# Performance work log

Hardware: AMD Instinct MI355X
Metric: run time of the kernel (lower is better)

The kernel has to match this reference:

```python
import jax, jax.numpy as jnp
import numpy as np

N, D_IN, HID, NH = 16384, 2048, 2048, 16
HD = HID // NH  # head_size = 128


def setup_inputs() -> dict:
    key = jax.random.key(0)
    ks = jax.random.split(key, 8)
    s = 1.0 / np.sqrt(D_IN)
    return {
        "protein": jax.random.normal(ks[0], (N, D_IN), jnp.float32),
        "drug": jax.random.normal(ks[1], (N, D_IN), jnp.float32),
        "mask_prot": jnp.ones((N,), bool),
        "mask_drug": jnp.ones((N,), bool),
        "Wq_p": jax.random.uniform(ks[2], (D_IN, HID), jnp.float32, -s, s),
        "Wk_p": jax.random.uniform(ks[3], (D_IN, HID), jnp.float32, -s, s),
        "Wv_p": jax.random.uniform(ks[4], (D_IN, HID), jnp.float32, -s, s),
        "Wq_d": jax.random.uniform(ks[5], (D_IN, HID), jnp.float32, -s, s),
        "Wk_d": jax.random.uniform(ks[6], (D_IN, HID), jnp.float32, -s, s),
        "Wv_d": jax.random.uniform(ks[7], (D_IN, HID), jnp.float32, -s, s),
    }


def _heads(x):
    # [N, L, HID] -> [N, L, NH, HD]
    return x.reshape(x.shape[0], x.shape[1], NH, HD)


def _alpha_logits(logits, mask_row, mask_col, inf=1e6):
    # logits: [N, L1, L2, H]; masks: [N, L1], [N, L2] (broadcast over heads)
    mask_pair = mask_row[:, :, None, None] & mask_col[:, None, :, None]
    logits = jnp.where(mask_pair, logits, logits - inf)
    alpha = jax.nn.softmax(logits, axis=2)
    alpha = jnp.where(mask_row[:, :, None, None], alpha, jnp.zeros_like(alpha))
    return alpha


def reference(protein, drug, mask_prot, mask_drug, Wq_p, Wk_p, Wv_p, Wq_d, Wk_d, Wv_d):
    p = protein[:, None, :]  # [N, 1, D_IN]
    d = drug[:, None, :]
    # forward() overwrites the masks with all-ones of shape [N, L=1]
    m_p = jnp.ones(p.shape[:-1], bool)
    m_d = jnp.ones(d.shape[:-1], bool)

    qp = _heads(jnp.einsum('bld,dh->blh', p, Wq_p))  # [N,1,NH,HD]
    kp = _heads(jnp.einsum('bld,dh->blh', p, Wk_p))
    vp = _heads(jnp.einsum('bld,dh->blh', p, Wv_p))
    qd = _heads(jnp.einsum('bld,dh->blh', d, Wq_d))
    kd = _heads(jnp.einsum('bld,dh->blh', d, Wk_d))
    vd = _heads(jnp.einsum('bld,dh->blh', d, Wv_d))

    logits_pp = jnp.einsum('blhd,bkhd->blkh', qp, kp)
    logits_pd = jnp.einsum('blhd,bkhd->blkh', qp, kd)
    logits_dp = jnp.einsum('blhd,bkhd->blkh', qd, kp)
    logits_dd = jnp.einsum('blhd,bkhd->blkh', qd, kd)

    a_pp = _alpha_logits(logits_pp, m_p, m_p)
    a_pd = _alpha_logits(logits_pd, m_p, m_d)
    a_dp = _alpha_logits(logits_dp, m_d, m_p)
    a_dd = _alpha_logits(logits_dd, m_d, m_d)

    def agg(alpha, v):
        out = jnp.einsum('blkh,bkhd->blhd', alpha, v)
        return out.reshape(out.shape[0], out.shape[1], HID)

    prot_embedding = (agg(a_pp, vp) + agg(a_pd, vd)) / 2  # [N,1,HID]
    drug_embedding = (agg(a_dp, vp) + agg(a_dd, vd)) / 2

    # agg_mode == 'cls'
    prot_embed = prot_embedding[:, 0]
    drug_embed = drug_embedding[:, 0]
    return jnp.concatenate([prot_embed, drug_embed], axis=1)  # [N, 2*HID]
```

## Files before the change

kernel.cpp:

```cpp
#include <hip/hip_runtime.h>
#include <stdint.h>


typedef __attribute__((ext_vector_type(8))) short short8;
typedef __attribute__((ext_vector_type(4))) float float4v;
typedef __attribute__((ext_vector_type(2))) unsigned int uint2v;

typedef const __attribute__((address_space(1))) unsigned int* gp_t;
typedef __attribute__((address_space(3))) unsigned int* lp_t;

#define M_DIM 16384
#define N_DIM 2048
#define K_DIM 4096
#define OUT_LD 4096

static __device__ __forceinline__ unsigned int pack_bf16x2(float x, float y) {
  union { float f; unsigned int u; } a, b;
  a.f = x; b.f = y;
  unsigned int ua = a.u + 0x8000u;
  unsigned int ub = b.u + 0x8000u;
  return __builtin_amdgcn_perm(ub, ua, 0x07060302u);
}

static __device__ __forceinline__ unsigned short f2bf(float x) {
  union { float f; unsigned int u; } a; a.f = x;
  return (unsigned short)((a.u + 0x8000u) >> 16);
}

__global__ __launch_bounds__(256)
void prep_wt(const float* __restrict__ Wp, const float* __restrict__ Wd,
             unsigned short* __restrict__ Wt) {
  __shared__ float tile[32][33];
  const int k0 = blockIdx.x * 32;
  const int n0 = blockIdx.y * 32;
  const int tx = threadIdx.x;
  const int ty = threadIdx.y;
  const float* W = (k0 < 2048) ? Wp : Wd;
  const int kk0 = (k0 < 2048) ? k0 : k0 - 2048;
#pragma unroll
  for (int i = 0; i < 4; ++i) {
    int r = ty * 4 + i;
    tile[r][tx] = W[(size_t)(kk0 + r) * 2048 + n0 + tx];
  }
  __syncthreads();
#pragma unroll
  for (int i = 0; i < 4; ++i) {
    int r = ty * 4 + i;
    Wt[(size_t)(n0 + r) * (size_t)K_DIM + k0 + tx] = f2bf(tile[tx][r]);
  }
}

__global__ __launch_bounds__(256)
void cast_a(const float* __restrict__ P, const float* __restrict__ Dg,
            unsigned int* __restrict__ Abf) {
  int idx = blockIdx.x * 256 + threadIdx.x;
  int row = idx >> 10;
  int j = (idx & 1023) << 2;
  const float* src = (j < 2048) ? (P + (size_t)row * 2048 + j)
                                : (Dg + (size_t)row * 2048 + (j - 2048));
  float4v v = *(const float4v*)src;
  uint2v o;
  o.x = pack_bf16x2(v.x, v.y);
  o.y = pack_bf16x2(v.z, v.w);
  *(uint2v*)(Abf + (size_t)row * 2048 + (j >> 1)) = o;
}

template <bool ABF>
__global__ __launch_bounds__(256)
void gemm_k(const unsigned int* __restrict__ Abf,
            const float* __restrict__ Ap, const float* __restrict__ Ad,
            const unsigned short* __restrict__ Wt,
            float* __restrict__ out) {
  __shared__ unsigned short As[128 * 64];
  __shared__ unsigned short Bs[128 * 64];

  const int t = threadIdx.x;
  const int bx = blockIdx.x;
  const int tn = bx & 15, tm = bx >> 4;
  const int m0 = tm << 7, n0 = tn << 7;
  const int w = t >> 6, l = t & 63;
  const int wm = w & 1, wn = w >> 1;
  const int lr = l & 15, q = l >> 4;

  const int rB = t >> 3;
  const int kB = (t & 7) * 8;

  float4v acc[4][4];
#pragma unroll
  for (int i = 0; i < 4; ++i)
#pragma unroll
    for (int j = 0; j < 4; ++j)
      acc[i][j] = (float4v){0.f, 0.f, 0.f, 0.f};

  for (int k0 = 0; k0 < K_DIM; k0 += 64) {
#pragma unroll
    for (int i = 0; i < 4; ++i) {
      const unsigned short* g =
          Wt + (size_t)(n0 + i * 32 + rB) * (size_t)K_DIM + (k0 + kB);
      __builtin_amdgcn_global_load_lds((gp_t)(const void*)g,
                                       (lp_t)&Bs[i * 2048 + w * 512], 16, 0, 0);
    }
    if constexpr (ABF) {
#pragma unroll
      for (int i = 0; i < 4; ++i) {
        const unsigned int* g =
            Abf + ((size_t)(m0 + i * 32 + rB) * (size_t)K_DIM + (k0 + kB)) / 2;
        __builtin_amdgcn_global_load_lds((gp_t)(const void*)g,
                                         (lp_t)&As[i * 2048 + w * 512], 16, 0, 0);
      }
    } else {
      const float* base;
      int kk;
      if (k0 < 2048) { base = Ap; kk = k0; } else { base = Ad; kk = k0 - 2048; }
      const int rA = t >> 4;
      const int cA = (t & 15) * 4;
#pragma unroll
      for (int i = 0; i < 8; ++i) {
        int m = i * 16 + rA;
        float4v v = *(const float4v*)(base + (size_t)(m0 + m) * 2048 + kk + cA);
        uint2v o;
        o.x = pack_bf16x2(v.x, v.y);
        o.y = pack_bf16x2(v.z, v.w);
        *(uint2v*)&As[m * 64 + cA] = o;
      }
    }
    __syncthreads();

#pragma unroll
    for (int ks = 0; ks < 2; ++ks) {
      short8 af[4], bfr[4];
#pragma unroll
      for (int i = 0; i < 4; ++i) {
        af[i]  = *(const short8*)&As[(wm * 64 + i * 16 + lr) * 64 + ks * 32 + q * 8];
        bfr[i] = *(const short8*)&Bs[(wn * 64 + i * 16 + lr) * 64 + ks * 32 + q * 8];
      }
#pragma unroll
      for (int i = 0; i < 4; ++i)
#pragma unroll
        for (int j = 0; j < 4; ++j)
          acc[i][j] = __builtin_amdgcn_mfma_f32_16x16x32_bf16(af[i], bfr[j],
                                                              acc[i][j], 0, 0, 0);
    }
    __syncthreads();
  }

#pragma unroll
  for (int i = 0; i < 4; ++i) {
    const int r0 = m0 + wm * 64 + i * 16 + q * 4;
#pragma unroll
    for (int j = 0; j < 4; ++j) {
      const int c = n0 + wn * 64 + j * 16 + lr;
#pragma unroll
      for (int r = 0; r < 4; ++r) {
        float v = acc[i][j][r] * 0.5f;
        size_t o = (size_t)(r0 + r) * (size_t)OUT_LD + c;
        out[o] = v;
        out[o + 2048] = v;
      }
    }
  }
}

__global__ __launch_bounds__(256)
void gemm_fallback(const float* __restrict__ P, const float* __restrict__ Dg,
                   const float* __restrict__ Wp, const float* __restrict__ Wd,
                   float* __restrict__ out) {
  __shared__ float Asf[64][17];
  __shared__ float Bsf[16][65];
  const int bx = blockIdx.x;
  const int by = blockIdx.y;
  const int t = threadIdx.x;
  const int tc = t & 15, trw = t >> 4;
  const int m0 = by * 64, n0 = bx * 64;
  float accf[4][4] = {};
  for (int k0 = 0; k0 < 4096; k0 += 16) {
    const float* Asrc = (k0 < 2048) ? P : Dg;
    const float* Bsrc = (k0 < 2048) ? Wp : Wd;
    const int kk = k0 & 2047;
#pragma unroll
    for (int i = 0; i < 4; ++i) {
      int r = i * 16 + trw;
      Asf[r][tc] = Asrc[(size_t)(m0 + r) * 2048 + kk + tc];
    }
#pragma unroll
    for (int i = 0; i < 4; ++i) {
      int r = i * 4 + (t >> 6);
      int c = t & 63;
      Bsf[r][c] = Bsrc[(size_t)(kk + r) * 2048 + n0 + c];
    }
    __syncthreads();
#pragma unroll
    for (int k2 = 0; k2 < 16; ++k2) {
      float a[4], b[4];
#pragma unroll
      for (int i = 0; i < 4; ++i) a[i] = Asf[trw * 4 + i][k2];
#pragma unroll
      for (int j = 0; j < 4; ++j) b[j] = Bsf[k2][tc * 4 + j];
#pragma unroll
      for (int i = 0; i < 4; ++i)
#pragma unroll
        for (int j = 0; j < 4; ++j) accf[i][j] += a[i] * b[j];
    }
    __syncthreads();
  }
#pragma unroll
  for (int i = 0; i < 4; ++i)
#pragma unroll
    for (int j = 0; j < 4; ++j) {
      float v = accf[i][j] * 0.5f;
      size_t o = (size_t)(m0 + trw * 4 + i) * 4096 + n0 + tc * 4 + j;
      out[o] = v;
      out[o + 2048] = v;
    }
}

extern "C" void kernel_launch(void* const* d_in, const int* in_sizes, int n_in,
                              void* d_out, int out_size, void* d_ws, size_t ws_size,
                              hipStream_t stream) {
  const float* protein = (const float*)d_in[0];
  const float* drug    = (const float*)d_in[1];
  const float* Wv_p    = (const float*)d_in[6];
  const float* Wv_d    = (const float*)d_in[9];
  float* out = (float*)d_out;

  const size_t wt_bytes = (size_t)N_DIM * K_DIM * sizeof(unsigned short);
  const size_t a_bytes  = (size_t)M_DIM * K_DIM * sizeof(unsigned short);

  if (ws_size >= wt_bytes) {
    unsigned short* Wt = (unsigned short*)d_ws;
    prep_wt<<<dim3(128, 64), dim3(32, 8), 0, stream>>>(Wv_p, Wv_d, Wt);
    if (ws_size >= wt_bytes + a_bytes) {
      unsigned int* Abf = (unsigned int*)((char*)d_ws + wt_bytes);
      cast_a<<<65536, 256, 0, stream>>>(protein, drug, Abf);
      gemm_k<true><<<2048, 256, 0, stream>>>(Abf, nullptr, nullptr, Wt, out);
    } else {
      gemm_k<false><<<2048, 256, 0, stream>>>(nullptr, protein, drug, Wt, out);
    }
  } else {
    gemm_fallback<<<dim3(32, 256), 256, 0, stream>>>(protein, drug, Wv_p, Wv_d, out);
  }
}
```

Before: 828.6 us.

## Fuse A fp32-to-bf16 cast into GEMM and XOR-swizzle LDS tiles

Drops the separate cast_a kernel and its bf16 A workspace round trip. The GEMM now loads fp32 A directly, converts it in registers and writes 16-byte chunks to LDS. Both the A and B LDS tiles use an XOR swizzle on the 8-element column chunk to avoid bank conflicts on the MFMA fragment reads. prep_wt now writes packed 4-element bf16 stores. The trade-off is that every output-column tile block reloads A as fp32, doubling A read traffic from L2/HBM, and A loads are synchronous rather than async global_load_lds.

```diff
diff --git a/kernel.cpp b/kernel.cpp
--- a/kernel.cpp
+++ b/kernel.cpp
@@ -5,6 +5,7 @@
 typedef __attribute__((ext_vector_type(8))) short short8;
 typedef __attribute__((ext_vector_type(4))) float float4v;
 typedef __attribute__((ext_vector_type(2))) unsigned int uint2v;
+typedef __attribute__((ext_vector_type(4))) unsigned int uint4v;
 
 typedef const __attribute__((address_space(1))) unsigned int* gp_t;
 typedef __attribute__((address_space(3))) unsigned int* lp_t;
@@ -17,9 +18,7 @@
 static __device__ __forceinline__ unsigned int pack_bf16x2(float x, float y) {
   union { float f; unsigned int u; } a, b;
   a.f = x; b.f = y;
-  unsigned int ua = a.u + 0x8000u;
-  unsigned int ub = b.u + 0x8000u;
-  return __builtin_amdgcn_perm(ub, ua, 0x07060302u);
+  return __builtin_amdgcn_perm(b.u + 0x8000u, a.u + 0x8000u, 0x07060302u);
 }
 
 static __device__ __forceinline__ unsigned short f2bf(float x) {
@@ -35,6 +34,7 @@
   const int n0 = blockIdx.y * 32;
   const int tx = threadIdx.x;
   const int ty = threadIdx.y;
+  const int t = ty * 32 + tx;
   const float* W = (k0 < 2048) ? Wp : Wd;
   const int kk0 = (k0 < 2048) ? k0 : k0 - 2048;
 #pragma unroll
@@ -43,32 +43,18 @@
     tile[r][tx] = W[(size_t)(kk0 + r) * 2048 + n0 + tx];
   }
   __syncthreads();
-#pragma unroll
-  for (int i = 0; i < 4; ++i) {
-    int r = ty * 4 + i;
-    Wt[(size_t)(n0 + r) * (size_t)K_DIM + k0 + tx] = f2bf(tile[tx][r]);
+  {
+    const int r = t >> 3;
+    const int c = (t & 7) * 4;
+    uint2v o;
+    o.x = pack_bf16x2(tile[c + 0][r], tile[c + 1][r]);
+    o.y = pack_bf16x2(tile[c + 2][r], tile[c + 3][r]);
+    *(uint2v*)&Wt[(size_t)(n0 + r) * (size_t)K_DIM + k0 + c] = o;
   }
 }
 
 __global__ __launch_bounds__(256)
-void cast_a(const float* __restrict__ P, const float* __restrict__ Dg,
-            unsigned int* __restrict__ Abf) {
-  int idx = blockIdx.x * 256 + threadIdx.x;
-  int row = idx >> 10;
-  int j = (idx & 1023) << 2;
-  const float* src = (j < 2048) ? (P + (size_t)row * 2048 + j)
-                                : (Dg + (size_t)row * 2048 + (j - 2048));
-  float4v v = *(const float4v*)src;
-  uint2v o;
-  o.x = pack_bf16x2(v.x, v.y);
-  o.y = pack_bf16x2(v.z, v.w);
-  *(uint2v*)(Abf + (size_t)row * 2048 + (j >> 1)) = o;
-}
-
-template <bool ABF>
-__global__ __launch_bounds__(256)
-void gemm_k(const unsigned int* __restrict__ Abf,
-            const float* __restrict__ Ap, const float* __restrict__ Ad,
+void gemm_f(const float* __restrict__ Ap, const float* __restrict__ Ad,
             const unsigned short* __restrict__ Wt,
             float* __restrict__ out) {
   __shared__ unsigned short As[128 * 64];
@@ -82,8 +68,9 @@
   const int wm = w & 1, wn = w >> 1;
   const int lr = l & 15, q = l >> 4;
 
-  const int rB = t >> 3;
-  const int kB = (t & 7) * 8;
+  const int rS = t >> 3;
+  const int cS = t & 7;
+  const int cSw = cS ^ (rS & 7);
 
   float4v acc[4][4];
 #pragma unroll
@@ -96,32 +83,26 @@
 #pragma unroll
     for (int i = 0; i < 4; ++i) {
       const unsigned short* g =
-          Wt + (size_t)(n0 + i * 32 + rB) * (size_t)K_DIM + (k0 + kB);
+          Wt + (size_t)(n0 + i * 32 + rS) * (size_t)K_DIM + k0 + cSw * 8;
       __builtin_amdgcn_global_load_lds((gp_t)(const void*)g,
                                        (lp_t)&Bs[i * 2048 + w * 512], 16, 0, 0);
     }
-    if constexpr (ABF) {
-#pragma unroll
-      for (int i = 0; i < 4; ++i) {
-        const unsigned int* g =
-            Abf + ((size_t)(m0 + i * 32 + rB) * (size_t)K_DIM + (k0 + kB)) / 2;
-        __builtin_amdgcn_global_load_lds((gp_t)(const void*)g,
-                                         (lp_t)&As[i * 2048 + w * 512], 16, 0, 0);
-      }
-    } else {
+    {
       const float* base;
       int kk;
       if (k0 < 2048) { base = Ap; kk = k0; } else { base = Ad; kk = k0 - 2048; }
-      const int rA = t >> 4;
-      const int cA = (t & 15) * 4;
-#pragma unroll
-      for (int i = 0; i < 8; ++i) {
-        int m = i * 16 + rA;
-        float4v v = *(const float4v*)(base + (size_t)(m0 + m) * 2048 + kk + cA);
-        uint2v o;
-        o.x = pack_bf16x2(v.x, v.y);
-        o.y = pack_bf16x2(v.z, v.w);
-        *(uint2v*)&As[m * 64 + cA] = o;
+#pragma unroll
+      for (int i = 0; i < 4; ++i) {
+        const int m = i * 32 + rS;
+        const float* src = base + (size_t)(m0 + m) * 2048 + kk + cS * 8;
+        float4v v0 = *(const float4v*)src;
+        float4v v1 = *(const float4v*)(src + 4);
+        uint4v o;
+        o.x = pack_bf16x2(v0.x, v0.y);
+        o.y = pack_bf16x2(v0.z, v0.w);
+        o.z = pack_bf16x2(v1.x, v1.y);
+        o.w = pack_bf16x2(v1.z, v1.w);
+        *(uint4v*)&As[m * 64 + (cS ^ (m & 7)) * 8] = o;
       }
     }
     __syncthreads();
@@ -131,8 +112,9 @@
       short8 af[4], bfr[4];
 #pragma unroll
       for (int i = 0; i < 4; ++i) {
-        af[i]  = *(const short8*)&As[(wm * 64 + i * 16 + lr) * 64 + ks * 32 + q * 8];
-        bfr[i] = *(const short8*)&Bs[(wn * 64 + i * 16 + lr) * 64 + ks * 32 + q * 8];
+        const int cw = ((ks * 4 + q) ^ (lr & 7)) * 8;
+        af[i]  = *(const short8*)&As[(wm * 64 + i * 16 + lr) * 64 + cw];
+        bfr[i] = *(const short8*)&Bs[(wn * 64 + i * 16 + lr) * 64 + cw];
       }
 #pragma unroll
       for (int i = 0; i < 4; ++i)
@@ -224,18 +206,11 @@
   float* out = (float*)d_out;
 
   const size_t wt_bytes = (size_t)N_DIM * K_DIM * sizeof(unsigned short);
-  const size_t a_bytes  = (size_t)M_DIM * K_DIM * sizeof(unsigned short);
 
   if (ws_size >= wt_bytes) {
     unsigned short* Wt = (unsigned short*)d_ws;
     prep_wt<<<dim3(128, 64), dim3(32, 8), 0, stream>>>(Wv_p, Wv_d, Wt);
-    if (ws_size >= wt_bytes + a_bytes) {
-      unsigned int* Abf = (unsigned int*)((char*)d_ws + wt_bytes);
-      cast_a<<<65536, 256, 0, stream>>>(protein, drug, Abf);
-      gemm_k<true><<<2048, 256, 0, stream>>>(Abf, nullptr, nullptr, Wt, out);
-    } else {
-      gemm_k<false><<<2048, 256, 0, stream>>>(nullptr, protein, drug, Wt, out);
-    }
+    gemm_f<<<2048, 256, 0, stream>>>(protein, drug, Wt, out);
   } else {
     gemm_fallback<<<dim3(32, 256), 256, 0, stream>>>(protein, drug, Wv_p, Wv_d, out);
   }
```

Result: slower. 891.2 us (+7.6%).
